# Kernel tuning notes

Hardware: AMD Instinct MI355X
Metric: run time of the kernel (lower is better)

Reference implementation:

```python
import jax, jax.numpy as jnp
import numpy as np

B, S, D, H = 2, 2048, 1024, 16
HD = D // H  # head_dim = 64


def setup_inputs() -> dict:
    key = jax.random.key(0)
    ks = jax.random.split(key, 9)
    sc = 1.0 / np.sqrt(D)
    return {
        "X": jax.random.normal(ks[0], (B, S, D), jnp.float32),
        "Wq": jax.random.normal(ks[1], (D, D), jnp.float32) * sc,
        "bq": jnp.zeros((D,), jnp.float32),
        "Wk": jax.random.normal(ks[2], (D, D), jnp.float32) * sc,
        "bk": jnp.zeros((D,), jnp.float32),
        "Wv": jax.random.normal(ks[3], (D, D), jnp.float32) * sc,
        "bv": jnp.zeros((D,), jnp.float32),
        "Wo": jax.random.normal(ks[4], (D, D), jnp.float32) * sc,
        "bo": jnp.zeros((D,), jnp.float32),
    }


def reference(X, Wq, bq, Wk, bk, Wv, bv, Wo, bo):
    b, s, d = X.shape
    q = (X @ Wq + bq).reshape(b, s, H, HD).transpose(0, 2, 1, 3)  # [B,H,S,HD]
    k = (X @ Wk + bk).reshape(b, s, H, HD).transpose(0, 2, 1, 3)
    v = (X @ Wv + bv).reshape(b, s, H, HD).transpose(0, 2, 1, 3)
    score = jnp.einsum("bhqd,bhkd->bhqk", q, k) / jnp.sqrt(jnp.float32(HD))
    causal = jnp.tril(jnp.ones((s, s), bool))  # [S,S]
    score = jnp.where(causal[None, None], score, -jnp.inf)
    attn = jax.nn.softmax(score, axis=-1)
    out = jnp.einsum("bhqk,bhkd->bhqd", attn, v)  # [B,H,S,HD]
    out = out.transpose(0, 2, 1, 3).reshape(b, s, d)
    return out @ Wo + bo
```

## Files before the change

kernel.cpp:

```cpp
#include <hip/hip_runtime.h>
#include <hip/hip_bf16.h>
#include <math.h>

#define B_SZ 2
#define S_SZ 2048
#define D_SZ 1024
#define H_SZ 16
#define HD_SZ 64
constexpr int M_ROWS = B_SZ * S_SZ;

typedef __bf16 bf16x8 __attribute__((ext_vector_type(8)));
typedef __bf16 bf16x4 __attribute__((ext_vector_type(4)));
typedef float f32x4 __attribute__((ext_vector_type(4)));

#define GLOAD_LDS16(gsrc, ldst)                                              \
  __builtin_amdgcn_global_load_lds(                                          \
      (const __attribute__((address_space(1))) void*)(gsrc),                 \
      (__attribute__((address_space(3))) void*)(ldst), 16, 0, 0)

__global__ __launch_bounds__(256) void prep_all(const float* __restrict__ X,
                                                const float* __restrict__ W0,
                                                const float* __restrict__ W1,
                                                const float* __restrict__ W2,
                                                const float* __restrict__ W3,
                                                __bf16* __restrict__ Xb,
                                                __bf16* __restrict__ Wt) {
  __shared__ float Ts[32][33];
  const int z = blockIdx.z;
  if (z < 4) {
    const float* W = z == 0 ? W0 : (z == 1 ? W1 : (z == 2 ? W2 : W3));
    __bf16* out = Wt + (size_t)z * 1024 * 1024;
    const int k0 = blockIdx.x * 32, n0 = blockIdx.y * 32;
    const int tr = threadIdx.x >> 3;
    const int tc = (threadIdx.x & 7) * 4;
    const float4 v =
        *reinterpret_cast<const float4*>(&W[(size_t)(k0 + tr) * 1024 + n0 + tc]);
    Ts[tr][tc + 0] = v.x;
    Ts[tr][tc + 1] = v.y;
    Ts[tr][tc + 2] = v.z;
    Ts[tr][tc + 3] = v.w;
    __syncthreads();
    bf16x4 o;
#pragma unroll
    for (int j = 0; j < 4; ++j) o[j] = (__bf16)Ts[tc + j][tr];
    *reinterpret_cast<bf16x4*>(&out[(size_t)(n0 + tr) * 1024 + k0 + tc]) = o;
  } else {
    const int flat = blockIdx.y * 32 + blockIdx.x;
    const size_t e0 = ((size_t)flat * 256 + threadIdx.x) * 16;
#pragma unroll
    for (int half = 0; half < 2; ++half) {
      const float4 a = *reinterpret_cast<const float4*>(&X[e0 + half * 8]);
      const float4 b = *reinterpret_cast<const float4*>(&X[e0 + half * 8 + 4]);
      bf16x8 o;
      o[0] = (__bf16)a.x; o[1] = (__bf16)a.y; o[2] = (__bf16)a.z; o[3] = (__bf16)a.w;
      o[4] = (__bf16)b.x; o[5] = (__bf16)b.y; o[6] = (__bf16)b.z; o[7] = (__bf16)b.w;
      *reinterpret_cast<bf16x8*>(&Xb[e0 + half * 8]) = o;
    }
  }
}

template <int MODE, int BN>
__global__ __launch_bounds__(256) void gemm_mfma(
    const __bf16* __restrict__ Ab, const __bf16* __restrict__ Bt,
    const float* __restrict__ bias0, const float* __restrict__ bias1,
    const float* __restrict__ bias2, float* __restrict__ C0,
    __bf16* __restrict__ Q0, __bf16* __restrict__ K0, __bf16* __restrict__ V0,
    int M, int N, int K) {
  constexpr int NJ = BN / 32;
  __shared__ __bf16 As[2][128 * 32];
  __shared__ __bf16 Bs[2][BN * 32];
  __shared__ __bf16 Ep[128 * 40];

  const int tid = threadIdx.x;
  const int lane = tid & 63;
  const int w = tid >> 6;
  const int lr = lane & 15, lg = lane >> 4;
  const int wr = w >> 1, wc = w & 1;
  const int bm = blockIdx.x * 128;
  const int bn = blockIdx.y * BN;

  const int r0 = tid >> 2, c0 = (tid & 3) * 8;
  const int r1 = (tid + 256) >> 2, c1 = ((tid + 256) & 3) * 8;
  const __bf16* aS0 = &Ab[(size_t)(bm + r0) * K + c0];
  const __bf16* aS1 = &Ab[(size_t)(bm + r1) * K + c1];
  const __bf16* bS0 = &Bt[(size_t)(bn + r0) * K + c0];
  const __bf16* bS1 = &Bt[(size_t)(bn + r1) * K + c1];

  f32x4 acc[4][NJ] = {};

  auto STAGE = [&](int buf) {
    GLOAD_LDS16(aS0, &As[buf][w * 512]);
    GLOAD_LDS16(aS1, &As[buf][2048 + w * 512]);
    GLOAD_LDS16(bS0, &Bs[buf][w * 512]);
    if constexpr (BN == 128) GLOAD_LDS16(bS1, &Bs[buf][2048 + w * 512]);
    aS0 += 32; aS1 += 32; bS0 += 32;
    if constexpr (BN == 128) bS1 += 32;
  };

  STAGE(0);
  asm volatile("s_waitcnt vmcnt(0)" ::: "memory");
  __builtin_amdgcn_s_barrier();
  __builtin_amdgcn_sched_barrier(0);
  int cur = 0;

  for (int k0 = 0; k0 < K; k0 += 32) {
    const bool has_next = (k0 + 32 < K);
    if (has_next) STAGE(cur ^ 1);
    if (k0) {
      if (has_next) {
        if constexpr (BN == 128)
          asm volatile("s_waitcnt vmcnt(4)" ::: "memory");
        else
          asm volatile("s_waitcnt vmcnt(3)" ::: "memory");
      } else {
        asm volatile("s_waitcnt vmcnt(0)" ::: "memory");
      }
      __builtin_amdgcn_s_barrier();
      __builtin_amdgcn_sched_barrier(0);
    }

    bf16x8 af[4], bfr[NJ];
#pragma unroll
    for (int i = 0; i < 4; ++i)
      af[i] = *reinterpret_cast<const bf16x8*>(&As[cur][(wr * 64 + i * 16 + lr) * 32 + lg * 8]);
#pragma unroll
    for (int j = 0; j < NJ; ++j)
      bfr[j] = *reinterpret_cast<const bf16x8*>(&Bs[cur][(wc * (BN / 2) + j * 16 + lr) * 32 + lg * 8]);
    __builtin_amdgcn_s_setprio(1);
#pragma unroll
    for (int i = 0; i < 4; ++i)
#pragma unroll
      for (int j = 0; j < NJ; ++j)
        acc[i][j] = __builtin_amdgcn_mfma_f32_16x16x32_bf16(af[i], bfr[j], acc[i][j], 0, 0, 0);
    __builtin_amdgcn_s_setprio(0);
    __builtin_amdgcn_sched_barrier(0);
    __builtin_amdgcn_s_barrier();
    cur ^= 1;
  }

  if (MODE == 0) {
    float* Epf = reinterpret_cast<float*>(&Ep[0]);
    float bias2r[2];
#pragma unroll
    for (int j = 0; j < 2; ++j)
      bias2r[j] = bias0[bn + wc * 32 + j * 16 + lr];
#pragma unroll
    for (int i = 0; i < 4; ++i) {
      __syncthreads();
#pragma unroll
      for (int j = 0; j < NJ; ++j) {
        const int colw = wc * 32 + j * 16 + lr;
#pragma unroll
        for (int r = 0; r < 4; ++r)
          Epf[(wr * 16 + lg * 4 + r) * 68 + colw] = acc[i][j][r] + bias2r[j];
      }
      __syncthreads();
#pragma unroll
      for (int u = 0; u < 2; ++u) {
        const int c = tid + u * 256;
        const int sr = c >> 4;
        const int off = (c & 15) * 4;
        const int m = bm + (sr >> 4) * 64 + i * 16 + (sr & 15);
        *reinterpret_cast<float4*>(&C0[(size_t)m * N + bn + off]) =
            *reinterpret_cast<const float4*>(&Epf[sr * 68 + off]);
      }
    }
  } else {
    const int which = bn >> 10;
    const float* bp = which == 0 ? bias0 : (which == 1 ? bias1 : bias2);
    const float scale = which == 0 ? 0.18033688011112042f : 1.0f;
    float bias4[4];
#pragma unroll
    for (int j = 0; j < 4; ++j)
      bias4[j] = bp[(bn & 1023) + wc * 64 + j * 16 + lr];

    if (which < 2) {
      __bf16* dst = which == 0 ? Q0 : K0;
#pragma unroll
      for (int i = 0; i < 4; ++i) {
        __syncthreads();
#pragma unroll
        for (int j = 0; j < 4; ++j) {
          const int colw = wc * 64 + j * 16 + lr;
#pragma unroll
          for (int r = 0; r < 4; ++r)
            Ep[(wr * 16 + lg * 4 + r) * 132 + colw] =
                (__bf16)((acc[i][j][r] + bias4[j]) * scale);
        }
        __syncthreads();
#pragma unroll
        for (int u = 0; u < 2; ++u) {
          const int c = tid + u * 256;
          const int er = c >> 4;
          const int off = (c & 15) * 8;
          const int m = bm + (er >> 4) * 64 + i * 16 + (er & 15);
          const int nn = (bn & 1023) + off;
          const int hh = nn >> 6, hd = nn & 63;
          const int bb = m >> 11, ss = m & (S_SZ - 1);
          *reinterpret_cast<bf16x8*>(
              &dst[(((size_t)(bb * H_SZ + hh)) * S_SZ + ss) * HD_SZ + hd]) =
              *reinterpret_cast<const bf16x8*>(&Ep[er * 132 + off]);
        }
      }
    } else {
#pragma unroll
      for (int i = 0; i < 4; ++i) {
        __syncthreads();
#pragma unroll
        for (int j = 0; j < 4; ++j) {
          const int colw = wc * 64 + j * 16 + lr;
#pragma unroll
          for (int r = 0; r < 4; ++r)
            Ep[colw * 40 + wr * 16 + lg * 4 + r] =
                (__bf16)(acc[i][j][r] + bias4[j]);
        }
        __syncthreads();
        const int col = tid & 127, r2 = tid >> 7;
        const int nn = (bn & 1023) + col;
        const int hh = nn >> 6, hd = nn & 63;
        const int m0 = bm + r2 * 64 + i * 16;
        const int bb = m0 >> 11, ss0 = m0 & (S_SZ - 1);
        __bf16* dstp =
            &V0[(((size_t)(bb * H_SZ + hh)) * HD_SZ + hd) * S_SZ + ss0];
        *reinterpret_cast<bf16x8*>(dstp) =
            *reinterpret_cast<const bf16x8*>(&Ep[col * 40 + r2 * 16]);
        *reinterpret_cast<bf16x8*>(dstp + 8) =
            *reinterpret_cast<const bf16x8*>(&Ep[col * 40 + r2 * 16 + 8]);
      }
    }
  }
}

__global__ __launch_bounds__(256) void attn_mfma(const __bf16* __restrict__ Q,
                                                 const __bf16* __restrict__ Kg,
                                                 const __bf16* __restrict__ Vtg,
                                                 __bf16* __restrict__ Aout) {
  constexpr int PST = 76;
  __shared__ __bf16 Ks[2][64 * 64];
  __shared__ __bf16 Vts[2][64 * 64];
  __shared__ __bf16 Ps[4][16 * PST];

  const int tid = threadIdx.x;
  const int lane = tid & 63;
  const int w = tid >> 6;
  const int lr = lane & 15;
  const int lg = lane >> 4;

  const int flat = blockIdx.x;
  const int g = flat >> 5;
  const int qb = (g < 16) ? (31 - g) : (g - 16);
  const int hb = flat & 31;
  const int h = hb >> 1, b = hb & 1;
  const size_t base = (size_t)(b * H_SZ + h) * S_SZ * HD_SZ;
  const int q0 = qb * 64 + w * 16;

  bf16x8 aq[2];
#pragma unroll
  for (int hh = 0; hh < 2; ++hh)
    aq[hh] = *reinterpret_cast<const bf16x8*>(
        &Q[base + (size_t)(q0 + lr) * 64 + hh * 32 + lg * 8]);

  const int srow = lane >> 3;
  const int schunk = (lane & 7) ^ srow;

  bf16x8 ones8;
#pragma unroll
  for (int j = 0; j < 8; ++j) ones8[j] = (__bf16)1.0f;

  f32x4 oacc[4] = {};
  f32x4 oacc_l = {};

  const int ntiles = qb + 1;

  const int rbA = w * 16, rbB = w * 16 + 8;
  const __bf16* kS0 = &Kg[base + (size_t)(rbA + srow) * 64 + schunk * 8];
  const __bf16* kS1 = &Kg[base + (size_t)(rbB + srow) * 64 + schunk * 8];
  const __bf16* vS0 = &Vtg[base + (size_t)(rbA + srow) * S_SZ + schunk * 8];
  const __bf16* vS1 = &Vtg[base + (size_t)(rbB + srow) * S_SZ + schunk * 8];

  auto ISSUE = [&](int buf) {
    GLOAD_LDS16(kS0, &Ks[buf][rbA * 64]);
    GLOAD_LDS16(kS1, &Ks[buf][rbB * 64]);
    GLOAD_LDS16(vS0, &Vts[buf][rbA * 64]);
    GLOAD_LDS16(vS1, &Vts[buf][rbB * 64]);
  };

  ISSUE(0);
  int cur = 0;

  for (int t0 = 0; t0 < ntiles; ++t0) {
    asm volatile("s_waitcnt vmcnt(0)" ::: "memory");
    __builtin_amdgcn_s_barrier();
    __builtin_amdgcn_sched_barrier(0);

    if (t0 + 1 < ntiles) {
      kS0 += 64 * 64; kS1 += 64 * 64;
      vS0 += 64;      vS1 += 64;
      ISSUE(cur ^ 1);
    }

    f32x4 s[4];
    __builtin_amdgcn_s_setprio(1);
#pragma unroll
    for (int t = 0; t < 4; ++t) {
      const int row = t * 16 + lr;
      const bf16x8 k0f = *reinterpret_cast<const bf16x8*>(
          &Ks[cur][row * 64 + ((lg ^ (lr & 7)) * 8)]);
      const bf16x8 k1f = *reinterpret_cast<const bf16x8*>(
          &Ks[cur][row * 64 + (((4 | lg) ^ (lr & 7)) * 8)]);
      f32x4 z = (f32x4){0.f, 0.f, 0.f, 0.f};
      z = __builtin_amdgcn_mfma_f32_16x16x32_bf16(k0f, aq[0], z, 0, 0, 0);
      z = __builtin_amdgcn_mfma_f32_16x16x32_bf16(k1f, aq[1], z, 0, 0, 0);
      s[t] = z;
    }
    __builtin_amdgcn_s_setprio(0);

    if (t0 == qb) {
      const int qrow = q0 + lr;
#pragma unroll
      for (int t = 0; t < 4; ++t) {
#pragma unroll
        for (int r = 0; r < 4; ++r) {
          const int key = t0 * 64 + t * 16 + lg * 4 + r;
          if (key > qrow) s[t][r] = -INFINITY;
        }
      }
    }

#pragma unroll
    for (int t = 0; t < 4; ++t) {
      float e0 = __builtin_amdgcn_exp2f(s[t][0]);
      float e1 = __builtin_amdgcn_exp2f(s[t][1]);
      float e2 = __builtin_amdgcn_exp2f(s[t][2]);
      float e3 = __builtin_amdgcn_exp2f(s[t][3]);
      unsigned int w0, w1;
      asm("v_cvt_pk_bf16_f32 %0, %1, %2" : "=v"(w0) : "v"(e0), "v"(e1));
      asm("v_cvt_pk_bf16_f32 %0, %1, %2" : "=v"(w1) : "v"(e2), "v"(e3));
      uint2 pk; pk.x = w0; pk.y = w1;
      *reinterpret_cast<uint2*>(&Ps[w][lr * PST + t * 16 + lg * 4]) = pk;
    }
    asm volatile("s_waitcnt lgkmcnt(0)" ::: "memory");
    __builtin_amdgcn_sched_barrier(0);

    __builtin_amdgcn_s_setprio(1);
#pragma unroll
    for (int kh = 0; kh < 2; ++kh) {
      const bf16x8 pa = *reinterpret_cast<const bf16x8*>(
          &Ps[w][lr * PST + kh * 32 + lg * 8]);
#pragma unroll
      for (int dc = 0; dc < 4; ++dc) {
        const int row = dc * 16 + lr;
        const bf16x8 vf = *reinterpret_cast<const bf16x8*>(
            &Vts[cur][row * 64 + (((kh * 4 + lg) ^ (lr & 7)) * 8)]);
        oacc[dc] = __builtin_amdgcn_mfma_f32_16x16x32_bf16(pa, vf, oacc[dc], 0, 0, 0);
      }
      oacc_l = __builtin_amdgcn_mfma_f32_16x16x32_bf16(pa, ones8, oacc_l, 0, 0, 0);
    }
    __builtin_amdgcn_s_setprio(0);
    __builtin_amdgcn_sched_barrier(0);
    cur ^= 1;
  }

#pragma unroll
  for (int r = 0; r < 4; ++r) {
    const float inv = 1.f / oacc_l[r];
#pragma unroll
    for (int dc = 0; dc < 4; ++dc)
      Ps[w][(lg * 4 + r) * PST + dc * 16 + lr] = (__bf16)(oacc[dc][r] * inv);
  }
  asm volatile("s_waitcnt lgkmcnt(0)" ::: "memory");
  __builtin_amdgcn_sched_barrier(0);
#pragma unroll
  for (int u = 0; u < 2; ++u) {
    const int c = lane + u * 64;
    const int row = c >> 3;
    const int off = (c & 7) * 8;
    const int qg = q0 + row;
    *reinterpret_cast<bf16x8*>(
        &Aout[(size_t)(b * S_SZ + qg) * D_SZ + h * 64 + off]) =
        *reinterpret_cast<const bf16x8*>(&Ps[w][row * PST + off]);
  }
}

extern "C" void kernel_launch(void* const* d_in, const int* in_sizes, int n_in,
                              void* d_out, int out_size, void* d_ws,
                              size_t ws_size, hipStream_t stream) {
  const float* X = (const float*)d_in[0];
  const float* Wq = (const float*)d_in[1];
  const float* bq = (const float*)d_in[2];
  const float* Wk = (const float*)d_in[3];
  const float* bk = (const float*)d_in[4];
  const float* Wv = (const float*)d_in[5];
  const float* bv = (const float*)d_in[6];
  const float* Wo = (const float*)d_in[7];
  const float* bo = (const float*)d_in[8];
  float* out = (float*)d_out;

  const size_t elems = (size_t)M_ROWS * D_SZ;
  const size_t welems = (size_t)D_SZ * D_SZ;
  __bf16* Xb = (__bf16*)d_ws;
  __bf16* Wt = Xb + elems;
  __bf16* Q = Wt + 4 * welems;
  __bf16* K = Q + elems;
  __bf16* Vt = K + elems;
  __bf16* Ahb = Vt + elems;

  prep_all<<<dim3(32, 32, 5), 256, 0, stream>>>(X, Wq, Wk, Wv, Wo, Xb, Wt);

  gemm_mfma<1, 128><<<dim3(M_ROWS / 128, 3072 / 128), 256, 0, stream>>>(
      Xb, Wt, bq, bk, bv, nullptr, Q, K, Vt, M_ROWS, 3072, D_SZ);

  attn_mfma<<<dim3(1024), 256, 0, stream>>>(Q, K, Vt, Ahb);

  gemm_mfma<0, 64><<<dim3(M_ROWS / 128, D_SZ / 64), 256, 0, stream>>>(
      Ahb, Wt + 3 * welems, bo, nullptr, nullptr, out, nullptr, nullptr,
      nullptr, M_ROWS, D_SZ, D_SZ);
}
```

Before: 102.9 us.

## Split long causal attention query blocks across two workgroups with a combine pass

The upper half of the query blocks (the longest causal KV ranges) is now split across two workgroups, each covering half of the KV tiles. Each piece writes unnormalized fp32 partial outputs and row sums to workspace, and a new combine kernel adds the pieces, normalizes and writes bf16. The grid grows from 1024 to 1536 blocks to balance work across CUs and shorten the tail. The cost is an extra kernel launch plus fp32 partial traffic through global memory. The partials can be summed directly because the kernel uses a fixed softmax offset with no running max.

```diff
diff --git a/kernel.cpp b/kernel.cpp
--- a/kernel.cpp
+++ b/kernel.cpp
@@ -231,10 +231,11 @@
   }
 }
 
-__global__ __launch_bounds__(256) void attn_mfma(const __bf16* __restrict__ Q,
-                                                 const __bf16* __restrict__ Kg,
-                                                 const __bf16* __restrict__ Vtg,
-                                                 __bf16* __restrict__ Aout) {
+__global__ __launch_bounds__(256) void attn_mfma(
+    const __bf16* __restrict__ Q, const __bf16* __restrict__ Kg,
+    const __bf16* __restrict__ Vtg, __bf16* __restrict__ Aout,
+    float* __restrict__ Op0, float* __restrict__ Op1,
+    float* __restrict__ lp0, float* __restrict__ lp1) {
   constexpr int PST = 76;
   __shared__ __bf16 Ks[2][64 * 64];
   __shared__ __bf16 Vts[2][64 * 64];
@@ -248,9 +249,22 @@
 
   const int flat = blockIdx.x;
   const int g = flat >> 5;
-  const int qb = (g < 16) ? (31 - g) : (g - 16);
   const int hb = flat & 31;
   const int h = hb >> 1, b = hb & 1;
+
+  int qb, tstart, tend, piece;
+  bool split;
+  if (g < 16) {
+    qb = 31 - g; split = true; piece = 0;
+    tstart = 0; tend = (qb + 2) >> 1;
+  } else if (g < 32) {
+    qb = 47 - g; split = true; piece = 1;
+    tstart = (qb + 2) >> 1; tend = qb + 1;
+  } else {
+    qb = 47 - g; split = false; piece = 0;
+    tstart = 0; tend = qb + 1;
+  }
+
   const size_t base = (size_t)(b * H_SZ + h) * S_SZ * HD_SZ;
   const int q0 = qb * 64 + w * 16;
 
@@ -270,13 +284,15 @@
   f32x4 oacc[4] = {};
   f32x4 oacc_l = {};
 
-  const int ntiles = qb + 1;
-
   const int rbA = w * 16, rbB = w * 16 + 8;
-  const __bf16* kS0 = &Kg[base + (size_t)(rbA + srow) * 64 + schunk * 8];
-  const __bf16* kS1 = &Kg[base + (size_t)(rbB + srow) * 64 + schunk * 8];
-  const __bf16* vS0 = &Vtg[base + (size_t)(rbA + srow) * S_SZ + schunk * 8];
-  const __bf16* vS1 = &Vtg[base + (size_t)(rbB + srow) * S_SZ + schunk * 8];
+  const __bf16* kS0 =
+      &Kg[base + ((size_t)tstart * 64 + rbA + srow) * 64 + schunk * 8];
+  const __bf16* kS1 =
+      &Kg[base + ((size_t)tstart * 64 + rbB + srow) * 64 + schunk * 8];
+  const __bf16* vS0 =
+      &Vtg[base + (size_t)(rbA + srow) * S_SZ + tstart * 64 + schunk * 8];
+  const __bf16* vS1 =
+      &Vtg[base + (size_t)(rbB + srow) * S_SZ + tstart * 64 + schunk * 8];
 
   auto ISSUE = [&](int buf) {
     GLOAD_LDS16(kS0, &Ks[buf][rbA * 64]);
@@ -288,12 +304,12 @@
   ISSUE(0);
   int cur = 0;
 
-  for (int t0 = 0; t0 < ntiles; ++t0) {
+  for (int t0 = tstart; t0 < tend; ++t0) {
     asm volatile("s_waitcnt vmcnt(0)" ::: "memory");
     __builtin_amdgcn_s_barrier();
     __builtin_amdgcn_sched_barrier(0);
 
-    if (t0 + 1 < ntiles) {
+    if (t0 + 1 < tend) {
       kS0 += 64 * 64; kS1 += 64 * 64;
       vS0 += 64;      vS1 += 64;
       ISSUE(cur ^ 1);
@@ -361,25 +377,83 @@
     cur ^= 1;
   }
 
-#pragma unroll
-  for (int r = 0; r < 4; ++r) {
-    const float inv = 1.f / oacc_l[r];
+  if (!split) {
+#pragma unroll
+    for (int r = 0; r < 4; ++r) {
+      const float inv = 1.f / oacc_l[r];
+#pragma unroll
+      for (int dc = 0; dc < 4; ++dc)
+        Ps[w][(lg * 4 + r) * PST + dc * 16 + lr] = (__bf16)(oacc[dc][r] * inv);
+    }
+    asm volatile("s_waitcnt lgkmcnt(0)" ::: "memory");
+    __builtin_amdgcn_sched_barrier(0);
+#pragma unroll
+    for (int u = 0; u < 2; ++u) {
+      const int c = lane + u * 64;
+      const int row = c >> 3;
+      const int off = (c & 7) * 8;
+      const int qg = q0 + row;
+      *reinterpret_cast<bf16x8*>(
+          &Aout[(size_t)(b * S_SZ + qg) * D_SZ + h * 64 + off]) =
+          *reinterpret_cast<const bf16x8*>(&Ps[w][row * PST + off]);
+    }
+  } else {
+    float* Op = piece ? Op1 : Op0;
+    float* lp = piece ? lp1 : lp0;
+    __syncthreads();
+    float* Ef = (w < 2)
+                    ? (reinterpret_cast<float*>(&Ks[0][0]) + w * 1088)
+                    : (reinterpret_cast<float*>(&Vts[0][0]) + (w - 2) * 1088);
 #pragma unroll
     for (int dc = 0; dc < 4; ++dc)
-      Ps[w][(lg * 4 + r) * PST + dc * 16 + lr] = (__bf16)(oacc[dc][r] * inv);
-  }
-  asm volatile("s_waitcnt lgkmcnt(0)" ::: "memory");
-  __builtin_amdgcn_sched_barrier(0);
-#pragma unroll
-  for (int u = 0; u < 2; ++u) {
-    const int c = lane + u * 64;
-    const int row = c >> 3;
-    const int off = (c & 7) * 8;
-    const int qg = q0 + row;
-    *reinterpret_cast<bf16x8*>(
-        &Aout[(size_t)(b * S_SZ + qg) * D_SZ + h * 64 + off]) =
-        *reinterpret_cast<const bf16x8*>(&Ps[w][row * PST + off]);
-  }
+#pragma unroll
+      for (int r = 0; r < 4; ++r)
+        Ef[(lg * 4 + r) * 68 + dc * 16 + lr] = oacc[dc][r];
+    asm volatile("s_waitcnt lgkmcnt(0)" ::: "memory");
+    __builtin_amdgcn_sched_barrier(0);
+    const size_t rbase = (size_t)hb * 1024 + (q0 - 1024);
+#pragma unroll
+    for (int u = 0; u < 4; ++u) {
+      const int c = u * 64 + lane;
+      const int row = c >> 4;
+      const int fo = (c & 15) * 4;
+      *reinterpret_cast<float4*>(&Op[(rbase + row) * 64 + fo]) =
+          *reinterpret_cast<const float4*>(&Ef[row * 68 + fo]);
+    }
+    if (lr == 0) {
+#pragma unroll
+      for (int r = 0; r < 4; ++r) lp[rbase + lg * 4 + r] = oacc_l[r];
+    }
+  }
+}
+
+__global__ __launch_bounds__(256) void combine_split(
+    const float* __restrict__ O0, const float* __restrict__ O1,
+    const float* __restrict__ l0, const float* __restrict__ l1,
+    __bf16* __restrict__ Ahb) {
+  const int t = blockIdx.x * 256 + threadIdx.x;
+  const int bh = t >> 13;
+  const int rem = t & 8191;
+  const int lrow = rem >> 3;
+  const int off = (rem & 7) * 8;
+  const size_t idx = ((size_t)bh * 1024 + lrow) * 64 + off;
+  const float4 a0 = *reinterpret_cast<const float4*>(&O0[idx]);
+  const float4 a1 = *reinterpret_cast<const float4*>(&O0[idx + 4]);
+  const float4 c0 = *reinterpret_cast<const float4*>(&O1[idx]);
+  const float4 c1 = *reinterpret_cast<const float4*>(&O1[idx + 4]);
+  const float inv = 1.f / (l0[bh * 1024 + lrow] + l1[bh * 1024 + lrow]);
+  bf16x8 o;
+  o[0] = (__bf16)((a0.x + c0.x) * inv);
+  o[1] = (__bf16)((a0.y + c0.y) * inv);
+  o[2] = (__bf16)((a0.z + c0.z) * inv);
+  o[3] = (__bf16)((a0.w + c0.w) * inv);
+  o[4] = (__bf16)((a1.x + c1.x) * inv);
+  o[5] = (__bf16)((a1.y + c1.y) * inv);
+  o[6] = (__bf16)((a1.z + c1.z) * inv);
+  o[7] = (__bf16)((a1.w + c1.w) * inv);
+  const int h = bh >> 1, b = bh & 1;
+  *reinterpret_cast<bf16x8*>(
+      &Ahb[((size_t)(b * S_SZ) + 1024 + lrow) * D_SZ + h * 64 + off]) = o;
 }
 
 extern "C" void kernel_launch(void* const* d_in, const int* in_sizes, int n_in,
@@ -404,13 +478,18 @@
   __bf16* K = Q + elems;
   __bf16* Vt = K + elems;
   __bf16* Ahb = Vt + elems;
+  float* Op0 = (float*)(Ahb + elems);
+  float* Op1 = Op0 + (size_t)32 * 1024 * 64;
+  float* lp0 = Op1 + (size_t)32 * 1024 * 64;
+  float* lp1 = lp0 + 32 * 1024;
 
   prep_all<<<dim3(32, 32, 5), 256, 0, stream>>>(X, Wq, Wk, Wv, Wo, Xb, Wt);
 
   gemm_mfma<1, 128><<<dim3(M_ROWS / 128, 3072 / 128), 256, 0, stream>>>(
       Xb, Wt, bq, bk, bv, nullptr, Q, K, Vt, M_ROWS, 3072, D_SZ);
 
-  attn_mfma<<<dim3(1024), 256, 0, stream>>>(Q, K, Vt, Ahb);
+  attn_mfma<<<dim3(1536), 256, 0, stream>>>(Q, K, Vt, Ahb, Op0, Op1, lp0, lp1);
+  combine_split<<<dim3(1024), 256, 0, stream>>>(Op0, Op1, lp0, lp1, Ahb);
 
   gemm_mfma<0, 64><<<dim3(M_ROWS / 128, D_SZ / 64), 256, 0, stream>>>(
       Ahb, Wt + 3 * welems, bo, nullptr, nullptr, out, nullptr, nullptr,
```

After: 108.3 us. +5.2%, slower.
